# Kernel optimization log

Hardware: AMD Instinct MI355X
Metric: run time of the kernel (lower is better)

The kernel has to match this reference:

```python
import jax, jax.numpy as jnp
import numpy as np

B, T = 32, 256
INPUT_DIM, TRAJ_TYPE_DIM = 10000, 32
HIDDEN, N_LAYERS, EMBED = 512, 2, 256
OUTPUT_DIM = 10000


def setup_inputs() -> dict:
    key = jax.random.key(0)
    ks = jax.random.split(key, 16)
    s = 0.05
    inp = {
        "locations": jax.random.randint(ks[0], (B, T), 0, INPUT_DIM),
        "times": jax.random.uniform(ks[1], (B, T, 1), dtype=jnp.float32),
        "labels": jax.random.randint(ks[2], (B,), 0, TRAJ_TYPE_DIM),
        "emb_table": jax.random.normal(ks[3], (INPUT_DIM, EMBED), jnp.float32) * s,
        "traj_emb": jax.random.normal(ks[4], (TRAJ_TYPE_DIM, HIDDEN * N_LAYERS), jnp.float32) * s,
        "w_ih0": jax.random.normal(ks[5], (3 * HIDDEN, EMBED + 1), jnp.float32) * s,
        "w_hh0": jax.random.normal(ks[6], (3 * HIDDEN, HIDDEN), jnp.float32) * s,
        "b_ih0": jax.random.normal(ks[7], (3 * HIDDEN,), jnp.float32) * s,
        "b_hh0": jax.random.normal(ks[8], (3 * HIDDEN,), jnp.float32) * s,
        "w_ih1": jax.random.normal(ks[9], (3 * HIDDEN, HIDDEN), jnp.float32) * s,
        "w_hh1": jax.random.normal(ks[10], (3 * HIDDEN, HIDDEN), jnp.float32) * s,
        "b_ih1": jax.random.normal(ks[11], (3 * HIDDEN,), jnp.float32) * s,
        "b_hh1": jax.random.normal(ks[12], (3 * HIDDEN,), jnp.float32) * s,
        "fc_w": jax.random.normal(ks[13], (OUTPUT_DIM + 1, HIDDEN), jnp.float32) * s,
        "fc_b": jax.random.normal(ks[14], (OUTPUT_DIM + 1,), jnp.float32) * s,
    }
    return inp


def _gru_layer(x_tbf, h0, w_ih, w_hh, b_ih, b_hh):
    # x_tbf: [T, B, F]; h0: [B, H]. Standard torch GRU cell math.
    x_gates = jnp.einsum("tbf,gf->tbg", x_tbf, w_ih) + b_ih  # [T,B,3H]

    def step(h, xg):
        hg = h @ w_hh.T + b_hh
        xr, xz, xn = jnp.split(xg, 3, axis=-1)
        hr, hz, hn = jnp.split(hg, 3, axis=-1)
        r = jax.nn.sigmoid(xr + hr)
        z = jax.nn.sigmoid(xz + hz)
        n = jnp.tanh(xn + r * hn)
        h_new = (1.0 - z) * n + z * h
        return h_new, h_new

    _, outs = jax.lax.scan(step, h0, x_gates)
    return outs  # [T, B, H]


def reference(locations, times, labels, emb_table, traj_emb,
              w_ih0, w_hh0, b_ih0, b_hh0, w_ih1, w_hh1, b_ih1, b_hh1,
              fc_w, fc_b):
    # init hidden: [B, L*H] -> flat view -> [L, B, H] (matches torch .view)
    h0 = traj_emb[labels].reshape(N_LAYERS, -1, HIDDEN)
    x = jnp.concatenate([emb_table[locations], times], axis=-1)  # [B,T,E+1]
    x = jnp.swapaxes(x, 0, 1)  # [T,B,E+1]
    x = _gru_layer(x, h0[0], w_ih0, w_hh0, b_ih0, b_hh0)
    x = _gru_layer(x, h0[1], w_ih1, w_hh1, b_ih1, b_hh1)
    out = jnp.swapaxes(x, 0, 1)  # [B,T,H]
    out = jax.nn.relu(out) @ fc_w.T + fc_b  # [B,T,OUT+1]
    location = jax.nn.log_softmax(out[:, :, :-1], axis=-1)
    time = jax.nn.sigmoid(out[:, :, -1])
    return (location, time)
```

## Files before the change

### kernel.cpp

```cpp
#include <hip/hip_runtime.h>

typedef unsigned short u16;
typedef __bf16 bf16x8 __attribute__((ext_vector_type(8)));
typedef float f32x4 __attribute__((ext_vector_type(4)));

#define DEVI __device__ __forceinline__

DEVI u16 f2b(float f) {
  union { float f; unsigned u; } c; c.f = f;
  unsigned r = c.u + 0x7FFFu + ((c.u >> 16) & 1u);
  return (u16)(r >> 16);
}

DEVI float sigm(float x) { return 1.f / (1.f + __expf(-x)); }
DEVI float tanhfast(float x) {
  x = fminf(fmaxf(x, -15.f), 15.f);
  float e = __expf(2.f * x);
  return (e - 1.f) / (e + 1.f);
}

DEVI void async16(const void* g, void* l) {
  __builtin_amdgcn_global_load_lds((const __attribute__((address_space(1))) void*)g,
                                   (__attribute__((address_space(3))) void*)l, 16, 0, 0);
}

DEVI f32x4 ld16cc(const u16* p) {
  f32x4 r;
  asm volatile("global_load_dwordx4 %0, %1, off sc0 sc1" : "=v"(r) : "v"(p) : "memory");
  return r;
}

#define VM0 asm volatile("s_waitcnt vmcnt(0)" ::: "memory")
#define SBAR __builtin_amdgcn_sched_barrier(0)

__global__ __launch_bounds__(256) void k_castpad(const float* __restrict__ src, u16* __restrict__ dst,
                                                 int srows, int scols, int drows, int dcols) {
  size_t n = (size_t)drows * dcols;
  for (size_t i = blockIdx.x * 256 + threadIdx.x; i < n; i += (size_t)gridDim.x * 256) {
    int r = (int)(i / dcols), c = (int)(i % dcols);
    float v = (r < srows && c < scols) ? src[(size_t)r * scols + c] : 0.f;
    dst[i] = f2b(v);
  }
}

__global__ __launch_bounds__(256) void k_embed(const int* __restrict__ loc, const float* __restrict__ times,
                                               const float* __restrict__ emb, u16* __restrict__ x0) {
  int m = blockIdx.x * 4 + (threadIdx.x >> 6);
  int s = threadIdx.x & 63;
  int b = m & 31, t = m >> 5;
  int li = loc[b * 256 + t];
  const float4* er = (const float4*)(emb + (size_t)li * 256);
  u16* xr = x0 + (size_t)m * 288;
  float4 v = er[s];
  ushort4 u;
  u.x = f2b(v.x); u.y = f2b(v.y); u.z = f2b(v.z); u.w = f2b(v.w);
  *(ushort4*)(xr + s * 4) = u;
  if (s == 0) xr[256] = f2b(times[b * 256 + t]);
  else if (s <= 31) xr[256 + s] = 0;
}

__global__ __launch_bounds__(256) void k_hinit(const float* __restrict__ traj, const int* __restrict__ labels,
                                               u16* __restrict__ dst, int layer) {
  int idx = blockIdx.x * 256 + threadIdx.x;
  if (idx < 16384) {
    int fidx = layer * 16384 + idx;
    dst[idx] = f2b(traj[(size_t)labels[fidx >> 10] * 1024 + (fidx & 1023)]);
  }
}

__global__ __launch_bounds__(128) void k_taginit(unsigned* __restrict__ tag0) {
  int t = threadIdx.x;
  tag0[(t >> 5) * 259 * 32 + (t & 31)] = 1u;
}

template <int MODE>
__global__ __launch_bounds__(256) void k_gemm(const u16* __restrict__ A, const u16* __restrict__ Bw,
                                              const float* __restrict__ bias, float* __restrict__ C,
                                              int N, int K, float* __restrict__ tptr) {
  __shared__ __align__(16) u16 As[128 * 32];
  __shared__ __align__(16) u16 Bs[128 * 32];
  const int tid = threadIdx.x;
  const int lane = tid & 63, wid = tid >> 6;
  const int tn = blockIdx.x, tm = blockIdx.y;
  const int wm = wid >> 1, wn = wid & 1;

  f32x4 acc[4][4] = {};

  const int r0 = tid >> 2;
  const int cb0 = (tid * 16) & 63;

  for (int k0 = 0; k0 < K; k0 += 32) {
    __syncthreads();
#pragma unroll
    for (int p = 0; p < 2; ++p) {
      int row = r0 + p * 64;
      const u16* ga = A + (size_t)(tm * 128 + row) * K + k0 + (cb0 >> 1);
      async16(ga, (void*)(As + wid * 512 + p * 2048));
      const u16* gb = Bw + (size_t)(tn * 128 + row) * K + k0 + (cb0 >> 1);
      async16(gb, (void*)(Bs + wid * 512 + p * 2048));
    }
    asm volatile("s_waitcnt vmcnt(0)" ::: "memory");
    __syncthreads();
    bf16x8 af[4], bf[4];
#pragma unroll
    for (int i = 0; i < 4; ++i) {
      af[i] = *reinterpret_cast<const bf16x8*>(As + (wm * 64 + i * 16 + (lane & 15)) * 32 + ((lane >> 4) * 8));
      bf[i] = *reinterpret_cast<const bf16x8*>(Bs + (wn * 64 + i * 16 + (lane & 15)) * 32 + ((lane >> 4) * 8));
    }
#pragma unroll
    for (int i = 0; i < 4; ++i)
#pragma unroll
      for (int j = 0; j < 4; ++j)
        acc[i][j] = __builtin_amdgcn_mfma_f32_16x16x32_bf16(af[i], bf[j], acc[i][j], 0, 0, 0);
  }

  const int row0 = tm * 128 + wm * 64;
  const int col0 = tn * 128 + wn * 64;
#pragma unroll
  for (int i = 0; i < 4; ++i)
#pragma unroll
    for (int j = 0; j < 4; ++j)
#pragma unroll
      for (int r = 0; r < 4; ++r) {
        int row = row0 + i * 16 + ((lane >> 4) * 4) + r;
        int col = col0 + j * 16 + (lane & 15);
        float v = acc[i][j][r];
        if (MODE == 0) {
          C[(size_t)row * N + col] = v + bias[col];
        } else {
          int orow = ((row & 31) << 8) + (row >> 5);
          if (col < 10000) C[(size_t)orow * 10000 + col] = v + bias[col];
          else if (col == 10000) tptr[orow] = sigm(v + bias[col]);
        }
      }
}

__global__ __launch_bounds__(512)
void k_scan9(const float* __restrict__ xg0,
             const u16* __restrict__ whh0, const float* __restrict__ bhh0,
             const u16* __restrict__ wih1, const float* __restrict__ bih1,
             const u16* __restrict__ whh1, const float* __restrict__ bhh1,
             const float* __restrict__ traj, const int* __restrict__ labels,
             u16* __restrict__ h0x, u16* __restrict__ h1x, float* __restrict__ x1x,
             u16* __restrict__ h1seq, unsigned* __restrict__ tag0, unsigned* __restrict__ tag1)
{
  extern __shared__ __align__(16) char dynlds[];
  float* smD = (float*)(dynlds + 98304);

  const int tid = threadIdx.x, bid = blockIdx.x;
  const int role = bid >> 5, blk = bid & 31;
  const int lane = tid & 63, wid = tid >> 6;
  const int rep = bid & 3;

  const int eb = tid >> 4, ejj = tid & 15;
  const int jg = (blk << 4) + ejj;

  const float* bhh = (role == 0) ? bhh0 : bhh1;
  int fidx = (role == 1 ? 16384 : 0) + eb * 512 + jg;
  float h_own = traj[(size_t)labels[fidx >> 10] * 1024 + (fidx & 1023)];
  const float bh_r = bhh[jg], bh_z = bhh[512 + jg], bh_n = bhh[1024 + jg];

  const int mt = (wid < 6) ? wid / 3 : 0, nt = (wid < 6) ? wid % 3 : 0;
  float bX = 0.f;
  if (wid < 6 && role == 0) bX = bih1[nt * 512 + (blk << 4) + (lane & 15)];

  {
    const u16* wh = (role == 0) ? whh0 : whh1;
    for (int c = tid; c < 3072; c += 512) {
      int row = c >> 6, o16 = c & 63;
      int grow = (row >> 4) * 512 + (blk << 4) + (row & 15);
      *(float4*)(dynlds + (row << 10) + ((o16 * 16) ^ ((row & 7) << 4))) =
          *(const float4*)(wh + (size_t)grow * 512 + o16 * 8);
    }
    if (role == 0) {
      for (int c = tid; c < 3072; c += 512) {
        int row = c >> 6, o16 = c & 63;
        int grow = (row >> 4) * 512 + (blk << 4) + (row & 15);
        *(float4*)(dynlds + 49152 + (row << 10) + ((o16 * 16) ^ ((row & 7) << 4))) =
            *(const float4*)(wih1 + (size_t)grow * 512 + o16 * 8);
      }
    }
  }
  __syncthreads();

  const u16* hsrc = (role == 0) ? h0x : h1x;
  u16* hdst = (role == 0) ? h0x : h1x;
  unsigned* mytag = (role == 0) ? tag0 : tag1;

  for (int s = 0; s < 258; ++s) {
    if (role == 0 && s == 257) break;
    const int rp = (s + 1) & 1, wp = s & 1;

    if (role == 0) {
      float gxr = 0.f, gxz = 0.f, gxn = 0.f;
      if (s < 256) {
        const float* q = xg0 + (size_t)s * 49152 + eb * 1536 + jg;
        gxr = q[0]; gxz = q[512]; gxn = q[1024];
      }
      {
        const unsigned* tp;
        if (lane < 32)       tp = tag0 + ((size_t)(rep * 259 + s)) * 32 + lane;
        else if (s >= 9)     tp = tag1 + ((size_t)(rep * 259 + (s - 6))) * 32 + (lane - 32);
        else                 tp = tag0 + ((size_t)(rep * 259 + s)) * 32 + (lane - 32);
        while (__ballot(__hip_atomic_load(tp, __ATOMIC_RELAXED, __HIP_MEMORY_SCOPE_AGENT) != 0u) != ~0ull) {}
      }
      if (wid < 6) {
        const u16* hs = hsrc + (rp << 14) + ((mt * 16 + (lane & 15)) << 9) + ((lane >> 4) * 8);
        f32x4 afr[16];
#pragma unroll
        for (int ks = 0; ks < 16; ++ks) afr[ks] = ld16cc(hs + ks * 32);
        VM0; SBAR;
        const int col = lane & 15, rb = (lane >> 4) << 2;
        const int cb = (lane >> 4) << 4;
        const int swz = (col & 7) << 4;
        const int rowoff = (nt * 16 + col) << 10;
        if (s < 256) {
          f32x4 a0 = {0.f, 0.f, 0.f, 0.f}, a1 = {0.f, 0.f, 0.f, 0.f};
#pragma unroll
          for (int ks = 0; ks < 8; ++ks) {
            bf16x8 w0 = *(const bf16x8*)(dynlds + rowoff + (((2 * ks) * 64 + cb) ^ swz));
            bf16x8 w1 = *(const bf16x8*)(dynlds + rowoff + (((2 * ks + 1) * 64 + cb) ^ swz));
            a0 = __builtin_amdgcn_mfma_f32_16x16x32_bf16(__builtin_bit_cast(bf16x8, afr[2 * ks]),     w0, a0, 0, 0, 0);
            a1 = __builtin_amdgcn_mfma_f32_16x16x32_bf16(__builtin_bit_cast(bf16x8, afr[2 * ks + 1]), w1, a1, 0, 0, 0);
          }
#pragma unroll
          for (int r = 0; r < 4; ++r)
            smD[(mt * 3 + nt) * 256 + (rb + r) * 16 + col] = a0[r] + a1[r];
        }
        if (s >= 1) {
          f32x4 c0 = {0.f, 0.f, 0.f, 0.f}, c1 = {0.f, 0.f, 0.f, 0.f};
#pragma unroll
          for (int ks = 0; ks < 8; ++ks) {
            bf16x8 w0 = *(const bf16x8*)(dynlds + 49152 + rowoff + (((2 * ks) * 64 + cb) ^ swz));
            bf16x8 w1 = *(const bf16x8*)(dynlds + 49152 + rowoff + (((2 * ks + 1) * 64 + cb) ^ swz));
            c0 = __builtin_amdgcn_mfma_f32_16x16x32_bf16(__builtin_bit_cast(bf16x8, afr[2 * ks]),     w0, c0, 0, 0, 0);
            c1 = __builtin_amdgcn_mfma_f32_16x16x32_bf16(__builtin_bit_cast(bf16x8, afr[2 * ks + 1]), w1, c1, 0, 0, 0);
          }
          float* xp = x1x + (size_t)((s - 1) & 7) * 49152;
#pragma unroll
          for (int r = 0; r < 4; ++r) {
            int ebr = mt * 16 + rb + r;
            __hip_atomic_store(xp + ((ebr * 3 + nt) << 9) + (blk << 4) + col,
                               c0[r] + c1[r] + bX, __ATOMIC_RELAXED, __HIP_MEMORY_SCOPE_AGENT);
          }
        }
      }
      __syncthreads();
      if (s < 256) {
        float Dr = smD[((eb >> 4) * 3 + 0) * 256 + (eb & 15) * 16 + ejj] + bh_r;
        float Dz = smD[((eb >> 4) * 3 + 1) * 256 + (eb & 15) * 16 + ejj] + bh_z;
        float Dn = smD[((eb >> 4) * 3 + 2) * 256 + (eb & 15) * 16 + ejj] + bh_n;
        float r = sigm(gxr + Dr);
        float z = sigm(gxz + Dz);
        float n = tanhfast(gxn + r * Dn);
        h_own = (1.f - z) * n + z * h_own;
        unsigned hv = f2b(h_own);
        unsigned oth = __shfl_xor(hv, 1);
        if (!(ejj & 1))
          __hip_atomic_store((unsigned*)(hdst + (wp << 14)) + (((eb << 9) + jg) >> 1),
                             hv | (oth << 16), __ATOMIC_RELAXED, __HIP_MEMORY_SCOPE_AGENT);
      }
    } else {
      if (s >= 2) {
        {
          const unsigned* tp = (lane < 32)
              ? tag0 + ((size_t)(rep * 259 + s)) * 32 + lane
              : tag1 + ((size_t)(rep * 259 + s)) * 32 + (lane - 32);
          while (__ballot(__hip_atomic_load(tp, __ATOMIC_RELAXED, __HIP_MEMORY_SCOPE_AGENT) != 0u) != ~0ull) {}
        }
        float* xp = x1x + (size_t)((s - 2) & 7) * 49152 + ((eb * 3) << 9) + jg;
        float gxr = __hip_atomic_load(xp,        __ATOMIC_RELAXED, __HIP_MEMORY_SCOPE_AGENT);
        float gxz = __hip_atomic_load(xp + 512,  __ATOMIC_RELAXED, __HIP_MEMORY_SCOPE_AGENT);
        float gxn = __hip_atomic_load(xp + 1024, __ATOMIC_RELAXED, __HIP_MEMORY_SCOPE_AGENT);
        if (wid < 6) {
          const u16* hs = hsrc + (rp << 14) + ((mt * 16 + (lane & 15)) << 9) + ((lane >> 4) * 8);
          f32x4 afr[16];
#pragma unroll
          for (int ks = 0; ks < 16; ++ks) afr[ks] = ld16cc(hs + ks * 32);
          VM0; SBAR;
          const int col = lane & 15, rb = (lane >> 4) << 2;
          const int cb = (lane >> 4) << 4;
          const int swz = (col & 7) << 4;
          const int rowoff = (nt * 16 + col) << 10;
          f32x4 a0 = {0.f, 0.f, 0.f, 0.f}, a1 = {0.f, 0.f, 0.f, 0.f};
#pragma unroll
          for (int ks = 0; ks < 8; ++ks) {
            bf16x8 w0 = *(const bf16x8*)(dynlds + rowoff + (((2 * ks) * 64 + cb) ^ swz));
            bf16x8 w1 = *(const bf16x8*)(dynlds + rowoff + (((2 * ks + 1) * 64 + cb) ^ swz));
            a0 = __builtin_amdgcn_mfma_f32_16x16x32_bf16(__builtin_bit_cast(bf16x8, afr[2 * ks]),     w0, a0, 0, 0, 0);
            a1 = __builtin_amdgcn_mfma_f32_16x16x32_bf16(__builtin_bit_cast(bf16x8, afr[2 * ks + 1]), w1, a1, 0, 0, 0);
          }
#pragma unroll
          for (int r = 0; r < 4; ++r)
            smD[(mt * 3 + nt) * 256 + (rb + r) * 16 + col] = a0[r] + a1[r];
        }
        __syncthreads();
        float Dr = smD[((eb >> 4) * 3 + 0) * 256 + (eb & 15) * 16 + ejj] + bh_r;
        float Dz = smD[((eb >> 4) * 3 + 1) * 256 + (eb & 15) * 16 + ejj] + bh_z;
        float Dn = smD[((eb >> 4) * 3 + 2) * 256 + (eb & 15) * 16 + ejj] + bh_n;
        float r = sigm(gxr + Dr);
        float z = sigm(gxz + Dz);
        float n = tanhfast(gxn + r * Dn);
        h_own = (1.f - z) * n + z * h_own;
        unsigned hv = f2b(h_own);
        unsigned oth = __shfl_xor(hv, 1);
        if (!(ejj & 1))
          __hip_atomic_store((unsigned*)(hdst + (wp << 14)) + (((eb << 9) + jg) >> 1),
                             hv | (oth << 16), __ATOMIC_RELAXED, __HIP_MEMORY_SCOPE_AGENT);
        h1seq[((size_t)((s - 2) * 32 + eb) << 9) + jg] = f2b(fmaxf(h_own, 0.f));
      }
    }
    asm volatile("s_waitcnt vmcnt(0)" ::: "memory");
    __syncthreads();
    if (tid == 0 && s < 257) {
#pragma unroll
      for (int r = 0; r < 4; ++r)
        __hip_atomic_store(mytag + ((size_t)(r * 259 + s + 1)) * 32 + blk, 1u,
                           __ATOMIC_RELAXED, __HIP_MEMORY_SCOPE_AGENT);
    }
  }
}

__global__ __launch_bounds__(256) void k_logsoftmax(float* __restrict__ out) {
  const int row = blockIdx.x, tid = threadIdx.x;
  float* p = out + (size_t)row * 10000;
  const int n_own = (tid < 16) ? 40 : 39;
  float v[40];
  float mx = -3.4e38f;
#pragma unroll
  for (int i = 0; i < 40; ++i)
    if (i < n_own) { v[i] = p[i * 256 + tid]; mx = fmaxf(mx, v[i]); }
  for (int o = 32; o; o >>= 1) mx = fmaxf(mx, __shfl_xor(mx, o));
  __shared__ float sm[4], ss[4];
  if ((tid & 63) == 0) sm[tid >> 6] = mx;
  __syncthreads();
  mx = fmaxf(fmaxf(sm[0], sm[1]), fmaxf(sm[2], sm[3]));
  float s = 0.f;
#pragma unroll
  for (int i = 0; i < 40; ++i)
    if (i < n_own) s += __expf(v[i] - mx);
  for (int o = 32; o; o >>= 1) s += __shfl_xor(s, o);
  if ((tid & 63) == 0) ss[tid >> 6] = s;
  __syncthreads();
  s = ss[0] + ss[1] + ss[2] + ss[3];
  float lse = mx + __logf(s);
#pragma unroll
  for (int i = 0; i < 40; ++i)
    if (i < n_own) p[i * 256 + tid] = v[i] - lse;
}

extern "C" void kernel_launch(void* const* d_in, const int* in_sizes, int n_in,
                              void* d_out, int out_size, void* d_ws, size_t ws_size,
                              hipStream_t stream) {
  (void)in_sizes; (void)n_in; (void)out_size;
  const int*   loc    = (const int*)  d_in[0];
  const float* times  = (const float*)d_in[1];
  const int*   labels = (const int*)  d_in[2];
  const float* emb    = (const float*)d_in[3];
  const float* traj   = (const float*)d_in[4];
  const float* w_ih0  = (const float*)d_in[5];
  const float* w_hh0  = (const float*)d_in[6];
  const float* b_ih0  = (const float*)d_in[7];
  const float* b_hh0  = (const float*)d_in[8];
  const float* w_ih1  = (const float*)d_in[9];
  const float* w_hh1  = (const float*)d_in[10];
  const float* b_ih1  = (const float*)d_in[11];
  const float* b_hh1  = (const float*)d_in[12];
  const float* fc_w   = (const float*)d_in[13];
  const float* fc_b   = (const float*)d_in[14];

  if (ws_size < 32000000) return;

  char* ws = (char*)d_ws;
  size_t off = 0;
  auto alloc = [&](size_t b) { size_t r = off; off += (b + 255) & ~(size_t)255; return r; };
  unsigned* tag0 = (unsigned*)(ws + alloc(4 * 259 * 32 * 4));
  unsigned* tag1 = (unsigned*)(ws + alloc(4 * 259 * 32 * 4));
  u16*   h0x   = (u16*)  (ws + alloc(2 * 32 * 512 * 2));
  u16*   h1x   = (u16*)  (ws + alloc(2 * 32 * 512 * 2));
  float* x1x   = (float*)(ws + alloc((size_t)8 * 32 * 3 * 512 * 4));
  u16*   x0    = (u16*)  (ws + alloc((size_t)8192 * 288 * 2));
  u16*   wih0b = (u16*)  (ws + alloc((size_t)1536 * 288 * 2));
  u16*   whh0b = (u16*)  (ws + alloc((size_t)1536 * 512 * 2));
  u16*   wih1b = (u16*)  (ws + alloc((size_t)1536 * 512 * 2));
  u16*   whh1b = (u16*)  (ws + alloc((size_t)1536 * 512 * 2));
  u16*   fcwb  = (u16*)  (ws + alloc((size_t)10112 * 512 * 2));
  u16*   h1seq = (u16*)  (ws + alloc((size_t)8192 * 512 * 2));

  float* outp = (float*)d_out;
  float* xg0  = outp;
  float* tptr = outp + 81920000;

  hipFuncSetAttribute((const void*)k_scan9, hipFuncAttributeMaxDynamicSharedMemorySize, 104448);

  hipMemsetAsync(tag0, 0, 2 * 4 * 259 * 32 * 4, stream);
  k_taginit<<<1, 128, 0, stream>>>(tag0);
  k_castpad<<<1024, 256, 0, stream>>>(w_ih0, wih0b, 1536, 257, 1536, 288);
  k_castpad<<<1024, 256, 0, stream>>>(w_hh0, whh0b, 1536, 512, 1536, 512);
  k_castpad<<<1024, 256, 0, stream>>>(w_ih1, wih1b, 1536, 512, 1536, 512);
  k_castpad<<<1024, 256, 0, stream>>>(w_hh1, whh1b, 1536, 512, 1536, 512);
  k_castpad<<<1024, 256, 0, stream>>>(fc_w, fcwb, 10001, 512, 10112, 512);
  k_embed<<<2048, 256, 0, stream>>>(loc, times, emb, x0);
  k_gemm<0><<<dim3(12, 64), 256, 0, stream>>>(x0, wih0b, b_ih0, xg0, 1536, 288, nullptr);
  k_hinit<<<64, 256, 0, stream>>>(traj, labels, h0x + 16384, 0);
  k_hinit<<<64, 256, 0, stream>>>(traj, labels, h1x + 16384, 1);
  k_scan9<<<64, 512, 104448, stream>>>(xg0, whh0b, b_hh0, wih1b, b_ih1, whh1b, b_hh1,
                                       traj, labels, h0x, h1x, x1x, h1seq, tag0, tag1);
  k_gemm<1><<<dim3(79, 64), 256, 0, stream>>>(h1seq, fcwb, fc_b, outp, 10112, 512, tptr);
  k_logsoftmax<<<8192, 256, 0, stream>>>(outp);
}
```

Before: 1.782 ms.

## Consolidate scan MFMA into two waves and pass layer-1 input gates as bf16

The recurrent scan kernel now runs the per-step matvec MFMAs on 2 waves, each covering all three gate tiles, where 6 waves each handled one tile before. The layer-1 input-gate exchange buffer now holds packed bf16 pairs written with cache-bypassing stores, and the bias is added on the consumer side. The intent is to halve the cross-block traffic and trim per-wave load overhead on the latency-critical recurrence. In exchange each active wave does three times the MFMA work serially, which lengthens the step's critical path, and the gate inputs lose precision.

```diff
diff --git a/kernel.cpp b/kernel.cpp
--- a/kernel.cpp
+++ b/kernel.cpp
@@ -10,6 +10,9 @@
   union { float f; unsigned u; } c; c.f = f;
   unsigned r = c.u + 0x7FFFu + ((c.u >> 16) & 1u);
   return (u16)(r >> 16);
+}
+DEVI float b2f(u16 u) {
+  union { unsigned u; float f; } c; c.u = ((unsigned)u) << 16; return c.f;
 }
 
 DEVI float sigm(float x) { return 1.f / (1.f + __expf(-x)); }
@@ -29,6 +32,7 @@
   asm volatile("global_load_dwordx4 %0, %1, off sc0 sc1" : "=v"(r) : "v"(p) : "memory");
   return r;
 }
+DEVI void st32_g(unsigned* p, unsigned v) { asm volatile("global_store_dword %0, %1, off sc0 sc1" :: "v"(p), "v"(v) : "memory"); }
 
 #define VM0 asm volatile("s_waitcnt vmcnt(0)" ::: "memory")
 #define SBAR __builtin_amdgcn_sched_barrier(0)
@@ -136,13 +140,13 @@
 }
 
 __global__ __launch_bounds__(512)
-void k_scan9(const float* __restrict__ xg0,
-             const u16* __restrict__ whh0, const float* __restrict__ bhh0,
-             const u16* __restrict__ wih1, const float* __restrict__ bih1,
-             const u16* __restrict__ whh1, const float* __restrict__ bhh1,
-             const float* __restrict__ traj, const int* __restrict__ labels,
-             u16* __restrict__ h0x, u16* __restrict__ h1x, float* __restrict__ x1x,
-             u16* __restrict__ h1seq, unsigned* __restrict__ tag0, unsigned* __restrict__ tag1)
+void k_scan10(const float* __restrict__ xg0,
+              const u16* __restrict__ whh0, const float* __restrict__ bhh0,
+              const u16* __restrict__ wih1, const float* __restrict__ bih1,
+              const u16* __restrict__ whh1, const float* __restrict__ bhh1,
+              const float* __restrict__ traj, const int* __restrict__ labels,
+              u16* __restrict__ h0x, u16* __restrict__ h1x, u16* __restrict__ x1xb,
+              u16* __restrict__ h1seq, unsigned* __restrict__ tag0, unsigned* __restrict__ tag1)
 {
   extern __shared__ __align__(16) char dynlds[];
   float* smD = (float*)(dynlds + 98304);
@@ -159,10 +163,7 @@
   int fidx = (role == 1 ? 16384 : 0) + eb * 512 + jg;
   float h_own = traj[(size_t)labels[fidx >> 10] * 1024 + (fidx & 1023)];
   const float bh_r = bhh[jg], bh_z = bhh[512 + jg], bh_n = bhh[1024 + jg];
-
-  const int mt = (wid < 6) ? wid / 3 : 0, nt = (wid < 6) ? wid % 3 : 0;
-  float bX = 0.f;
-  if (wid < 6 && role == 0) bX = bih1[nt * 512 + (blk << 4) + (lane & 15)];
+  const float bi1r = bih1[jg], bi1z = bih1[512 + jg], bi1n = bih1[1024 + jg];
 
   {
     const u16* wh = (role == 0) ? whh0 : whh1;
@@ -204,44 +205,55 @@
         else                 tp = tag0 + ((size_t)(rep * 259 + s)) * 32 + (lane - 32);
         while (__ballot(__hip_atomic_load(tp, __ATOMIC_RELAXED, __HIP_MEMORY_SCOPE_AGENT) != 0u) != ~0ull) {}
       }
-      if (wid < 6) {
-        const u16* hs = hsrc + (rp << 14) + ((mt * 16 + (lane & 15)) << 9) + ((lane >> 4) * 8);
+      if (wid < 2) {
+        const int mt = wid;
+        const int col = lane & 15, hi = lane >> 4, rb = hi << 2;
+        const int cb = hi << 4;
+        const int swz = (col & 7) << 4;
+        const u16* hs = hsrc + (rp << 14) + ((mt * 16 + col) << 9) + (hi * 8);
         f32x4 afr[16];
 #pragma unroll
         for (int ks = 0; ks < 16; ++ks) afr[ks] = ld16cc(hs + ks * 32);
         VM0; SBAR;
-        const int col = lane & 15, rb = (lane >> 4) << 2;
-        const int cb = (lane >> 4) << 4;
-        const int swz = (col & 7) << 4;
-        const int rowoff = (nt * 16 + col) << 10;
         if (s < 256) {
-          f32x4 a0 = {0.f, 0.f, 0.f, 0.f}, a1 = {0.f, 0.f, 0.f, 0.f};
-#pragma unroll
-          for (int ks = 0; ks < 8; ++ks) {
-            bf16x8 w0 = *(const bf16x8*)(dynlds + rowoff + (((2 * ks) * 64 + cb) ^ swz));
-            bf16x8 w1 = *(const bf16x8*)(dynlds + rowoff + (((2 * ks + 1) * 64 + cb) ^ swz));
-            a0 = __builtin_amdgcn_mfma_f32_16x16x32_bf16(__builtin_bit_cast(bf16x8, afr[2 * ks]),     w0, a0, 0, 0, 0);
-            a1 = __builtin_amdgcn_mfma_f32_16x16x32_bf16(__builtin_bit_cast(bf16x8, afr[2 * ks + 1]), w1, a1, 0, 0, 0);
+#pragma unroll
+          for (int nt = 0; nt < 3; ++nt) {
+            const int rowoff = (nt * 16 + col) << 10;
+            f32x4 a0 = {0.f, 0.f, 0.f, 0.f}, a1 = {0.f, 0.f, 0.f, 0.f};
+#pragma unroll
+            for (int ks = 0; ks < 8; ++ks) {
+              bf16x8 w0 = *(const bf16x8*)(dynlds + rowoff + (((2 * ks) * 64 + cb) ^ swz));
+              bf16x8 w1 = *(const bf16x8*)(dynlds + rowoff + (((2 * ks + 1) * 64 + cb) ^ swz));
+              a0 = __builtin_amdgcn_mfma_f32_16x16x32_bf16(__builtin_bit_cast(bf16x8, afr[2 * ks]),     w0, a0, 0, 0, 0);
+              a1 = __builtin_amdgcn_mfma_f32_16x16x32_bf16(__builtin_bit_cast(bf16x8, afr[2 * ks + 1]), w1, a1, 0, 0, 0);
+            }
+#pragma unroll
+            for (int r = 0; r < 4; ++r)
+              smD[(mt * 3 + nt) * 256 + (rb + r) * 16 + col] = a0[r] + a1[r];
           }
-#pragma unroll
-          for (int r = 0; r < 4; ++r)
-            smD[(mt * 3 + nt) * 256 + (rb + r) * 16 + col] = a0[r] + a1[r];
         }
         if (s >= 1) {
-          f32x4 c0 = {0.f, 0.f, 0.f, 0.f}, c1 = {0.f, 0.f, 0.f, 0.f};
-#pragma unroll
-          for (int ks = 0; ks < 8; ++ks) {
-            bf16x8 w0 = *(const bf16x8*)(dynlds + 49152 + rowoff + (((2 * ks) * 64 + cb) ^ swz));
-            bf16x8 w1 = *(const bf16x8*)(dynlds + 49152 + rowoff + (((2 * ks + 1) * 64 + cb) ^ swz));
-            c0 = __builtin_amdgcn_mfma_f32_16x16x32_bf16(__builtin_bit_cast(bf16x8, afr[2 * ks]),     w0, c0, 0, 0, 0);
-            c1 = __builtin_amdgcn_mfma_f32_16x16x32_bf16(__builtin_bit_cast(bf16x8, afr[2 * ks + 1]), w1, c1, 0, 0, 0);
-          }
-          float* xp = x1x + (size_t)((s - 1) & 7) * 49152;
-#pragma unroll
-          for (int r = 0; r < 4; ++r) {
-            int ebr = mt * 16 + rb + r;
-            __hip_atomic_store(xp + ((ebr * 3 + nt) << 9) + (blk << 4) + col,
-                               c0[r] + c1[r] + bX, __ATOMIC_RELAXED, __HIP_MEMORY_SCOPE_AGENT);
+          u16* xp = x1xb + (size_t)((s - 1) & 7) * 49152;
+#pragma unroll
+          for (int nt = 0; nt < 3; ++nt) {
+            const int rowoff = (nt * 16 + col) << 10;
+            f32x4 c0 = {0.f, 0.f, 0.f, 0.f}, c1 = {0.f, 0.f, 0.f, 0.f};
+#pragma unroll
+            for (int ks = 0; ks < 8; ++ks) {
+              bf16x8 w0 = *(const bf16x8*)(dynlds + 49152 + rowoff + (((2 * ks) * 64 + cb) ^ swz));
+              bf16x8 w1 = *(const bf16x8*)(dynlds + 49152 + rowoff + (((2 * ks + 1) * 64 + cb) ^ swz));
+              c0 = __builtin_amdgcn_mfma_f32_16x16x32_bf16(__builtin_bit_cast(bf16x8, afr[2 * ks]),     w0, c0, 0, 0, 0);
+              c1 = __builtin_amdgcn_mfma_f32_16x16x32_bf16(__builtin_bit_cast(bf16x8, afr[2 * ks + 1]), w1, c1, 0, 0, 0);
+            }
+#pragma unroll
+            for (int r = 0; r < 4; ++r) {
+              int ebr = mt * 16 + rb + r;
+              unsigned hv = f2b(c0[r] + c1[r]);
+              unsigned oth = __shfl_xor(hv, 1);
+              if (!(col & 1))
+                st32_g((unsigned*)xp + (size_t)(ebr * 3 + nt) * 256 + (blk << 3) + (col >> 1),
+                       hv | (oth << 16));
+            }
           }
         }
       }
@@ -268,31 +280,38 @@
               : tag1 + ((size_t)(rep * 259 + s)) * 32 + (lane - 32);
           while (__ballot(__hip_atomic_load(tp, __ATOMIC_RELAXED, __HIP_MEMORY_SCOPE_AGENT) != 0u) != ~0ull) {}
         }
-        float* xp = x1x + (size_t)((s - 2) & 7) * 49152 + ((eb * 3) << 9) + jg;
-        float gxr = __hip_atomic_load(xp,        __ATOMIC_RELAXED, __HIP_MEMORY_SCOPE_AGENT);
-        float gxz = __hip_atomic_load(xp + 512,  __ATOMIC_RELAXED, __HIP_MEMORY_SCOPE_AGENT);
-        float gxn = __hip_atomic_load(xp + 1024, __ATOMIC_RELAXED, __HIP_MEMORY_SCOPE_AGENT);
-        if (wid < 6) {
-          const u16* hs = hsrc + (rp << 14) + ((mt * 16 + (lane & 15)) << 9) + ((lane >> 4) * 8);
+        const unsigned* xp = (const unsigned*)(x1xb + (size_t)((s - 2) & 7) * 49152);
+        unsigned dr = __hip_atomic_load(xp + (size_t)(eb * 3 + 0) * 256 + (jg >> 1), __ATOMIC_RELAXED, __HIP_MEMORY_SCOPE_AGENT);
+        unsigned dz = __hip_atomic_load(xp + (size_t)(eb * 3 + 1) * 256 + (jg >> 1), __ATOMIC_RELAXED, __HIP_MEMORY_SCOPE_AGENT);
+        unsigned dn = __hip_atomic_load(xp + (size_t)(eb * 3 + 2) * 256 + (jg >> 1), __ATOMIC_RELAXED, __HIP_MEMORY_SCOPE_AGENT);
+        float gxr = b2f((u16)((jg & 1) ? (dr >> 16) : dr)) + bi1r;
+        float gxz = b2f((u16)((jg & 1) ? (dz >> 16) : dz)) + bi1z;
+        float gxn = b2f((u16)((jg & 1) ? (dn >> 16) : dn)) + bi1n;
+        if (wid < 2) {
+          const int mt = wid;
+          const int col = lane & 15, hi = lane >> 4, rb = hi << 2;
+          const int cb = hi << 4;
+          const int swz = (col & 7) << 4;
+          const u16* hs = hsrc + (rp << 14) + ((mt * 16 + col) << 9) + (hi * 8);
           f32x4 afr[16];
 #pragma unroll
           for (int ks = 0; ks < 16; ++ks) afr[ks] = ld16cc(hs + ks * 32);
           VM0; SBAR;
-          const int col = lane & 15, rb = (lane >> 4) << 2;
-          const int cb = (lane >> 4) << 4;
-          const int swz = (col & 7) << 4;
-          const int rowoff = (nt * 16 + col) << 10;
-          f32x4 a0 = {0.f, 0.f, 0.f, 0.f}, a1 = {0.f, 0.f, 0.f, 0.f};
-#pragma unroll
-          for (int ks = 0; ks < 8; ++ks) {
-            bf16x8 w0 = *(const bf16x8*)(dynlds + rowoff + (((2 * ks) * 64 + cb) ^ swz));
-            bf16x8 w1 = *(const bf16x8*)(dynlds + rowoff + (((2 * ks + 1) * 64 + cb) ^ swz));
-            a0 = __builtin_amdgcn_mfma_f32_16x16x32_bf16(__builtin_bit_cast(bf16x8, afr[2 * ks]),     w0, a0, 0, 0, 0);
-            a1 = __builtin_amdgcn_mfma_f32_16x16x32_bf16(__builtin_bit_cast(bf16x8, afr[2 * ks + 1]), w1, a1, 0, 0, 0);
+#pragma unroll
+          for (int nt = 0; nt < 3; ++nt) {
+            const int rowoff = (nt * 16 + col) << 10;
+            f32x4 a0 = {0.f, 0.f, 0.f, 0.f}, a1 = {0.f, 0.f, 0.f, 0.f};
+#pragma unroll
+            for (int ks = 0; ks < 8; ++ks) {
+              bf16x8 w0 = *(const bf16x8*)(dynlds + rowoff + (((2 * ks) * 64 + cb) ^ swz));
+              bf16x8 w1 = *(const bf16x8*)(dynlds + rowoff + (((2 * ks + 1) * 64 + cb) ^ swz));
+              a0 = __builtin_amdgcn_mfma_f32_16x16x32_bf16(__builtin_bit_cast(bf16x8, afr[2 * ks]),     w0, a0, 0, 0, 0);
+              a1 = __builtin_amdgcn_mfma_f32_16x16x32_bf16(__builtin_bit_cast(bf16x8, afr[2 * ks + 1]), w1, a1, 0, 0, 0);
+            }
+#pragma unroll
+            for (int r = 0; r < 4; ++r)
+              smD[(mt * 3 + nt) * 256 + (rb + r) * 16 + col] = a0[r] + a1[r];
           }
-#pragma unroll
-          for (int r = 0; r < 4; ++r)
-            smD[(mt * 3 + nt) * 256 + (rb + r) * 16 + col] = a0[r] + a1[r];
         }
         __syncthreads();
         float Dr = smD[((eb >> 4) * 3 + 0) * 256 + (eb & 15) * 16 + ejj] + bh_r;
@@ -378,7 +397,7 @@
   unsigned* tag1 = (unsigned*)(ws + alloc(4 * 259 * 32 * 4));
   u16*   h0x   = (u16*)  (ws + alloc(2 * 32 * 512 * 2));
   u16*   h1x   = (u16*)  (ws + alloc(2 * 32 * 512 * 2));
-  float* x1x   = (float*)(ws + alloc((size_t)8 * 32 * 3 * 512 * 4));
+  u16*   x1xb  = (u16*)  (ws + alloc((size_t)8 * 32 * 3 * 512 * 2));
   u16*   x0    = (u16*)  (ws + alloc((size_t)8192 * 288 * 2));
   u16*   wih0b = (u16*)  (ws + alloc((size_t)1536 * 288 * 2));
   u16*   whh0b = (u16*)  (ws + alloc((size_t)1536 * 512 * 2));
@@ -391,7 +410,7 @@
   float* xg0  = outp;
   float* tptr = outp + 81920000;
 
-  hipFuncSetAttribute((const void*)k_scan9, hipFuncAttributeMaxDynamicSharedMemorySize, 104448);
+  hipFuncSetAttribute((const void*)k_scan10, hipFuncAttributeMaxDynamicSharedMemorySize, 104448);
 
   hipMemsetAsync(tag0, 0, 2 * 4 * 259 * 32 * 4, stream);
   k_taginit<<<1, 128, 0, stream>>>(tag0);
@@ -404,8 +423,8 @@
   k_gemm<0><<<dim3(12, 64), 256, 0, stream>>>(x0, wih0b, b_ih0, xg0, 1536, 288, nullptr);
   k_hinit<<<64, 256, 0, stream>>>(traj, labels, h0x + 16384, 0);
   k_hinit<<<64, 256, 0, stream>>>(traj, labels, h1x + 16384, 1);
-  k_scan9<<<64, 512, 104448, stream>>>(xg0, whh0b, b_hh0, wih1b, b_ih1, whh1b, b_hh1,
-                                       traj, labels, h0x, h1x, x1x, h1seq, tag0, tag1);
+  k_scan10<<<64, 512, 104448, stream>>>(xg0, whh0b, b_hh0, wih1b, b_ih1, whh1b, b_hh1,
+                                        traj, labels, h0x, h1x, x1xb, h1seq, tag0, tag1);
   k_gemm<1><<<dim3(79, 64), 256, 0, stream>>>(h1seq, fcwb, fc_b, outp, 10112, 512, tptr);
   k_logsoftmax<<<8192, 256, 0, stream>>>(outp);
 }
```

Result: no change. 1.786 ms (+0.2%).
